# Kernel optimization log

Measured on AMD Instinct MI355X. Metric: run time of the kernel, lower is better.

## Reference

```python
import math
import jax, jax.numpy as jnp
import numpy as np

B, H, S, D = 8, 16, 1024, 64
NEG = -1000000000.0


def setup_inputs() -> dict:
    key = jax.random.key(0)
    kq, kk, kv, km = jax.random.split(key, 4)
    return {
        "query": jax.random.normal(kq, (B, H, S, D), dtype=jnp.float32),
        "key": jax.random.normal(kk, (B, H, S, D), dtype=jnp.float32),
        "value": jax.random.normal(kv, (B, H, S, D), dtype=jnp.float32),
        "mask": jax.random.randint(km, (B, 1, S, S), 0, 2, dtype=jnp.int32),
    }


def reference(query, key, value, mask):
    dk = query.shape[-1]
    # [B,H,S,S] scores
    scores = jnp.einsum("bhqd,bhkd->bhqk", query, key) / math.sqrt(dk)
    valid = mask != 0  # broadcast [B,1,S,S]
    scores = jnp.where(valid, scores, NEG)
    attention = jax.nn.softmax(scores, axis=-1)
    # second masking pass: zero out masked attention weights
    attention = jnp.where(valid, attention, 0.0)
    out = jnp.einsum("bhqk,bhkd->bhqd", attention, value)
    return (out, attention)
```

## Files before the change

kernel.cpp:

```cpp
#include <hip/hip_runtime.h>
#include <stdint.h>


typedef _Float16 half8 __attribute__((ext_vector_type(8)));
typedef _Float16 half4v __attribute__((ext_vector_type(4)));
typedef float floatx4 __attribute__((ext_vector_type(4)));
typedef unsigned short u16;

constexpr int Bc = 8, Hc = 16, Sc = 1024, Dc = 64;
constexpr float NEGV = -1000000000.0f;
constexpr float SCALE = 0.125f;

__device__ inline half8 cvt8(float4 a, float4 b) {
    half8 h;
    h[0] = (_Float16)a.x; h[1] = (_Float16)a.y; h[2] = (_Float16)a.z; h[3] = (_Float16)a.w;
    h[4] = (_Float16)b.x; h[5] = (_Float16)b.y; h[6] = (_Float16)b.z; h[7] = (_Float16)b.w;
    return h;
}

__device__ inline void gll16(const void* g, void* l) {
    __builtin_amdgcn_global_load_lds(
        (const __attribute__((address_space(1))) unsigned int*)g,
        (__attribute__((address_space(3))) unsigned int*)l, 16, 0, 0);
}

__global__ __launch_bounds__(256) void prep_all(
    const float* __restrict__ K, const float* __restrict__ V,
    const int* __restrict__ M,
    _Float16* __restrict__ Kh, _Float16* __restrict__ Vh, u16* __restrict__ MB)
{
    const int bid = blockIdx.x;
    const int t = threadIdx.x;
    if (bid < 2048) {
        const size_t nv = (size_t)Bc * Hc * Sc * Dc / 4;
        for (size_t i = (size_t)bid * 256 + t; i < 2 * nv; i += (size_t)2048 * 256) {
            const bool isK = i < nv;
            const size_t j = isK ? i : i - nv;
            const float4 f = ((const float4*)(isK ? K : V))[j];
            half4v h;
            h[0] = (_Float16)f.x; h[1] = (_Float16)f.y;
            h[2] = (_Float16)f.z; h[3] = (_Float16)f.w;
            *(half4v*)((isK ? Kh : Vh) + j * 4) = h;
        }
    } else {
        const int id = bid - 2048;
        const int qt = id & 63, b = id >> 6;
        const int idx2 = t & 63;
        const int w2 = idx2 >> 4, cc = idx2 & 15;
        const int kbase = cc * 64 + w2 * 16;
#pragma unroll
        for (int it = 0; it < 4; ++it) {
            const int row = it * 4 + (t >> 6);
            const int* mp = M + ((size_t)b * Sc + qt * 16 + row) * Sc + kbase;
            unsigned m = 0;
#pragma unroll
            for (int j4 = 0; j4 < 4; ++j4) {
                const int4 mi = *(const int4*)(mp + j4 * 4);
                m |= (mi.x != 0 ? 1u : 0u) << (j4 * 4 + 0);
                m |= (mi.y != 0 ? 1u : 0u) << (j4 * 4 + 1);
                m |= (mi.z != 0 ? 1u : 0u) << (j4 * 4 + 2);
                m |= (mi.w != 0 ? 1u : 0u) << (j4 * 4 + 3);
            }
            MB[(size_t)(b * 64 + qt) * 1024 + row * 64 + idx2] = (u16)m;
        }
    }
}

__global__ __launch_bounds__(256, 3) void attn15(
    const float* __restrict__ Q,
    const _Float16* __restrict__ Kh, const _Float16* __restrict__ Vh,
    const u16* __restrict__ MB,
    float* __restrict__ Out, float* __restrict__ Attn)
{
    __shared__ __align__(16) unsigned char sh[49664];
    _Float16* p_lds      = (_Float16*)sh;
    unsigned char* stg   = sh + 32768;
    float* redM          = (float*)(sh + 49152);
    float* redS          = (float*)(sh + 49408);

    const int t = threadIdx.x, lane = t & 63, w = t >> 6;
    const int g = lane >> 4, n = lane & 15;
    const int bh = blockIdx.y, b = bh >> 4, qt = blockIdx.x, qtile = qt * 16;

    const unsigned char* KhB = (const unsigned char*)(Kh + (size_t)bh * Sc * Dc);
    const unsigned char* VhB = (const unsigned char*)(Vh + (size_t)bh * Sc * Dc);

    union { uint4 v[2]; u16 h[16]; } mu;
    {
        const u16* mrow = MB + (size_t)(b * 64 + qt) * 1024 + n * 64 + w * 16;
        mu.v[0] = *(const uint4*)&mrow[0];
        mu.v[1] = *(const uint4*)&mrow[8];
    }

    half8 qf0, qf1;
    {
        const float* qr = Q + ((size_t)bh * Sc + qtile + n) * Dc;
        float4 a0 = *(const float4*)&qr[g * 8];
        float4 a1 = *(const float4*)&qr[g * 8 + 4];
        float4 a2 = *(const float4*)&qr[32 + g * 8];
        float4 a3 = *(const float4*)&qr[32 + g * 8 + 4];
        a0.x *= SCALE; a0.y *= SCALE; a0.z *= SCALE; a0.w *= SCALE;
        a1.x *= SCALE; a1.y *= SCALE; a1.z *= SCALE; a1.w *= SCALE;
        a2.x *= SCALE; a2.y *= SCALE; a2.z *= SCALE; a2.w *= SCALE;
        a3.x *= SCALE; a3.y *= SCALE; a3.z *= SCALE; a3.w *= SCALE;
        qf0 = cvt8(a0, a1);
        qf1 = cvt8(a2, a3);
    }

    int koff[2], voff[2];
#pragma unroll
    for (int i = 0; i < 2; ++i) {
        const int G = w * 128 + i * 64 + lane;
        const int row = G >> 3, cb = (G & 7) * 16;
        koff[i] = row * 128 + (cb ^ ((row & 7) << 4));
        const int Gv = (i * 4 + w) * 64 + lane;
        const int st = Gv >> 3, jj = Gv & 7;
        const int jk = jj >> 1, dd8 = jj & 1;
        const int kb = st >> 5, d0 = (st >> 3) & 3, sub = (st >> 2) & 1, gg = st & 3;
        const int kk = kb * 32 + gg * 8 + sub * 4 + jk;
        voff[i] = kk * 128 + (d0 * 16 + dd8 * 8) * 2;
    }

    gll16(KhB + koff[0],        stg + w * 2048);
    gll16(KhB + koff[1],        stg + w * 2048 + 1024);
    gll16(KhB + 8192 + koff[0], stg + 8192 + w * 2048);
    gll16(KhB + 8192 + koff[1], stg + 8192 + w * 2048 + 1024);

    const int rowk = w * 16 + n;
    const int swk = (rowk & 7) << 4;
    float s[64];

#pragma unroll
    for (int c = 0; c < 16; ++c) {
        if (c == 15) { asm volatile("s_waitcnt vmcnt(0)" ::: "memory"); }
        else         { asm volatile("s_waitcnt vmcnt(2)" ::: "memory"); }
        __builtin_amdgcn_sched_barrier(0);
        const unsigned char* buf = stg + (c & 1) * 8192;
        const half8 kf0 = *(const half8*)(buf + rowk * 128 + ((g * 16) ^ swk));
        const half8 kf1 = *(const half8*)(buf + rowk * 128 + ((64 + g * 16) ^ swk));
        floatx4 acc = {0.f, 0.f, 0.f, 0.f};
        acc = __builtin_amdgcn_mfma_f32_16x16x32_f16(kf0, qf0, acc, 0, 0, 0);
        acc = __builtin_amdgcn_mfma_f32_16x16x32_f16(kf1, qf1, acc, 0, 0, 0);
        const unsigned mb = mu.h[c];
#pragma unroll
        for (int r = 0; r < 4; ++r)
            s[c * 4 + r] = ((mb >> (g * 4 + r)) & 1) ? acc[r] : NEGV;
        if (c + 2 < 16) {
            asm volatile("s_waitcnt lgkmcnt(0)" ::: "memory");
            __builtin_amdgcn_sched_barrier(0);
            unsigned char* dst = stg + (c & 1) * 8192 + w * 2048;
            gll16(KhB + (size_t)(c + 2) * 8192 + koff[0], dst);
            gll16(KhB + (size_t)(c + 2) * 8192 + koff[1], dst + 1024);
        }
    }

    float mloc = -3.4e38f;
#pragma unroll
    for (int c = 0; c < 16; ++c) {
        mloc = fmaxf(mloc, fmaxf(fmaxf(s[c * 4], s[c * 4 + 1]),
                                 fmaxf(s[c * 4 + 2], s[c * 4 + 3])));
    }
    mloc = fmaxf(mloc, __shfl_xor(mloc, 16, 64));
    mloc = fmaxf(mloc, __shfl_xor(mloc, 32, 64));
    if (lane < 16) redM[w * 16 + n] = mloc;
    __syncthreads();
    const float mx = fmaxf(fmaxf(redM[n], redM[16 + n]),
                           fmaxf(redM[32 + n], redM[48 + n]));

    gll16(VhB + voff[0],        stg + w * 1024);
    gll16(VhB + voff[1],        stg + (4 + w) * 1024);
    gll16(VhB + 8192 + voff[0], stg + 8192 + w * 1024);
    gll16(VhB + 8192 + voff[1], stg + 8192 + (4 + w) * 1024);

    float s0 = 0.f, s1 = 0.f, s2 = 0.f, s3 = 0.f;
#pragma unroll
    for (int c = 0; c < 16; ++c) {
        const float p0 = __expf(s[c * 4 + 0] - mx);
        const float p1 = __expf(s[c * 4 + 1] - mx);
        const float p2 = __expf(s[c * 4 + 2] - mx);
        const float p3 = __expf(s[c * 4 + 3] - mx);
        s[c * 4 + 0] = p0; s[c * 4 + 1] = p1;
        s[c * 4 + 2] = p2; s[c * 4 + 3] = p3;
        s0 += p0; s1 += p1; s2 += p2; s3 += p3;
    }
    float sloc = (s0 + s1) + (s2 + s3);
    sloc += __shfl_xor(sloc, 16, 64);
    sloc += __shfl_xor(sloc, 32, 64);
    if (lane < 16) redS[w * 16 + n] = sloc;
    __syncthreads();
    const float inv = __builtin_amdgcn_rcpf(redS[n] + redS[16 + n] +
                                            redS[32 + n] + redS[48 + n]);

    const unsigned swzn = (unsigned)((n & 7) << 3);
#pragma unroll
    for (int c = 0; c < 16; ++c) {
        const int col = c * 64 + w * 16 + g * 4;
        half4v hp;
        hp[0] = (_Float16)(s[c * 4 + 0] * inv);
        hp[1] = (_Float16)(s[c * 4 + 1] * inv);
        hp[2] = (_Float16)(s[c * 4 + 2] * inv);
        hp[3] = (_Float16)(s[c * 4 + 3] * inv);
        *(half4v*)&p_lds[n * 1024 + (col ^ swzn)] = hp;
    }
    __syncthreads();

    floatx4 oacc = {0.f, 0.f, 0.f, 0.f};

#pragma unroll
    for (int c = 0; c < 16; ++c) {
        if (c == 15) { asm volatile("s_waitcnt vmcnt(0)" ::: "memory"); }
        else         { asm volatile("s_waitcnt vmcnt(2)" ::: "memory"); }
        __builtin_amdgcn_sched_barrier(0);
        const unsigned vt_base = (unsigned)(uintptr_t)(stg + (c & 1) * 8192);
        __builtin_amdgcn_s_setprio(1);
        const int pc0 = c * 64 + g * 8;
        const half8 pa0 = *(const half8*)&p_lds[n * 1024 + (pc0 ^ swzn)];
        const half8 pa1 = *(const half8*)&p_lds[n * 1024 + ((pc0 + 32) ^ swzn)];
        const unsigned va0 = vt_base + (((unsigned)w * 8 + (unsigned)g) * 64 + (unsigned)n * 4) * 2;
        const unsigned va1 = va0 + 4096;
        half4v r0, r1, r2, r3;
        asm volatile("ds_read_b64_tr_b16 %0, %4\n\t"
                     "ds_read_b64_tr_b16 %1, %4 offset:512\n\t"
                     "ds_read_b64_tr_b16 %2, %5\n\t"
                     "ds_read_b64_tr_b16 %3, %5 offset:512"
                     : "=&v"(r0), "=&v"(r1), "=&v"(r2), "=&v"(r3)
                     : "v"(va0), "v"(va1));
        asm volatile("s_waitcnt lgkmcnt(0)" ::: "memory");
        __builtin_amdgcn_sched_barrier(0);
        if (c + 2 < 16) {
            unsigned char* dst = stg + (c & 1) * 8192;
            gll16(VhB + (size_t)(c + 2) * 8192 + voff[0], dst + w * 1024);
            gll16(VhB + (size_t)(c + 2) * 8192 + voff[1], dst + (4 + w) * 1024);
        }
        half8 vf0, vf1;
        vf0[0] = r0[0]; vf0[1] = r0[1]; vf0[2] = r0[2]; vf0[3] = r0[3];
        vf0[4] = r1[0]; vf0[5] = r1[1]; vf0[6] = r1[2]; vf0[7] = r1[3];
        vf1[0] = r2[0]; vf1[1] = r2[1]; vf1[2] = r2[2]; vf1[3] = r2[3];
        vf1[4] = r3[0]; vf1[5] = r3[1]; vf1[6] = r3[2]; vf1[7] = r3[3];
        oacc = __builtin_amdgcn_mfma_f32_16x16x32_f16(pa0, vf0, oacc, 0, 0, 0);
        oacc = __builtin_amdgcn_mfma_f32_16x16x32_f16(pa1, vf1, oacc, 0, 0, 0);
        __builtin_amdgcn_s_setprio(0);
    }

    const int dcol = w * 16 + n;
    const int qrow = qtile + g * 4;
    float* Ob = Out + (size_t)bh * Sc * Dc;
#pragma unroll
    for (int r = 0; r < 4; ++r) {
        __builtin_nontemporal_store(oacc[r], &Ob[(size_t)(qrow + r) * Dc + dcol]);
    }

    const int row_a = t >> 4, ca = (t & 15) * 4;
    const unsigned swza = (unsigned)((row_a & 7) << 3);
    float* arow = Attn + (size_t)bh * Sc * Sc + (size_t)(qtile + row_a) * Sc;
#pragma unroll
    for (int c = 0; c < 16; ++c) {
        const int col = c * 64 + ca;
        const half4v h = *(const half4v*)&p_lds[row_a * 1024 + (col ^ swza)];
        floatx4 f;
        f[0] = (float)h[0]; f[1] = (float)h[1]; f[2] = (float)h[2]; f[3] = (float)h[3];
        __builtin_nontemporal_store(f, (floatx4*)&arow[col]);
    }
}

__global__ __launch_bounds__(256, 4) void attn_fb(
    const float* __restrict__ Q, const float* __restrict__ K,
    const float* __restrict__ V, const int* __restrict__ M,
    float* __restrict__ Out, float* __restrict__ Attn)
{
    __shared__ __align__(16) unsigned char sh[33280];
    _Float16* p_lds = (_Float16*)sh;
    float*    redM  = (float*)(sh + 32768);
    float*    redS  = (float*)(sh + 33024);

    const int t = threadIdx.x, lane = t & 63, w = t >> 6;
    const int g = lane >> 4, n = lane & 15;
    const int bh = blockIdx.y, b = bh >> 4, qt = blockIdx.x, qtile = qt * 16;
    const int kbase = w * 256;

    half8 qf0, qf1;
    {
        const float* qr = Q + ((size_t)bh * Sc + qtile + n) * Dc;
        float4 a0 = *(const float4*)&qr[g * 8];
        float4 a1 = *(const float4*)&qr[g * 8 + 4];
        float4 a2 = *(const float4*)&qr[32 + g * 8];
        float4 a3 = *(const float4*)&qr[32 + g * 8 + 4];
        a0.x *= SCALE; a0.y *= SCALE; a0.z *= SCALE; a0.w *= SCALE;
        a1.x *= SCALE; a1.y *= SCALE; a1.z *= SCALE; a1.w *= SCALE;
        a2.x *= SCALE; a2.y *= SCALE; a2.z *= SCALE; a2.w *= SCALE;
        a3.x *= SCALE; a3.y *= SCALE; a3.z *= SCALE; a3.w *= SCALE;
        qf0 = cvt8(a0, a1);
        qf1 = cvt8(a2, a3);
    }

    float s[64];
#pragma unroll
    for (int kt = 0; kt < 16; ++kt) {
        const int key = kbase + kt * 16 + n;
        const float* kr = K + ((size_t)bh * Sc + key) * Dc;
        const half8 kf0 = cvt8(*(const float4*)&kr[g * 8], *(const float4*)&kr[g * 8 + 4]);
        const half8 kf1 = cvt8(*(const float4*)&kr[32 + g * 8], *(const float4*)&kr[32 + g * 8 + 4]);
        floatx4 acc = {0.f, 0.f, 0.f, 0.f};
        acc = __builtin_amdgcn_mfma_f32_16x16x32_f16(kf0, qf0, acc, 0, 0, 0);
        acc = __builtin_amdgcn_mfma_f32_16x16x32_f16(kf1, qf1, acc, 0, 0, 0);
        const int4 mi = *(const int4*)(M + ((size_t)b * Sc + qtile + n) * Sc +
                                       kbase + kt * 16 + g * 4);
        s[kt * 4 + 0] = mi.x ? acc[0] : NEGV;
        s[kt * 4 + 1] = mi.y ? acc[1] : NEGV;
        s[kt * 4 + 2] = mi.z ? acc[2] : NEGV;
        s[kt * 4 + 3] = mi.w ? acc[3] : NEGV;
    }

    float mloc = -3.4e38f;
#pragma unroll
    for (int kt = 0; kt < 16; ++kt)
        mloc = fmaxf(mloc, fmaxf(fmaxf(s[kt * 4], s[kt * 4 + 1]),
                                 fmaxf(s[kt * 4 + 2], s[kt * 4 + 3])));
    mloc = fmaxf(mloc, __shfl_xor(mloc, 16, 64));
    mloc = fmaxf(mloc, __shfl_xor(mloc, 32, 64));
    if (lane < 16) redM[w * 16 + n] = mloc;
    __syncthreads();
    const float mx = fmaxf(fmaxf(redM[n], redM[16 + n]),
                           fmaxf(redM[32 + n], redM[48 + n]));
    float sloc = 0.f;
#pragma unroll
    for (int kt = 0; kt < 16; ++kt) {
#pragma unroll
        for (int r = 0; r < 4; ++r) {
            const float p = __expf(s[kt * 4 + r] - mx);
            s[kt * 4 + r] = p;
            sloc += p;
        }
    }
    sloc += __shfl_xor(sloc, 16, 64);
    sloc += __shfl_xor(sloc, 32, 64);
    if (lane < 16) redS[w * 16 + n] = sloc;
    __syncthreads();
    const float inv = __builtin_amdgcn_rcpf(redS[n] + redS[16 + n] +
                                            redS[32 + n] + redS[48 + n]);

    const unsigned swzn = (unsigned)((n & 7) << 3);
#pragma unroll
    for (int kt = 0; kt < 16; ++kt) {
        const int col = kbase + kt * 16 + g * 4;
        half4v hp;
        hp[0] = (_Float16)(s[kt * 4 + 0] * inv);
        hp[1] = (_Float16)(s[kt * 4 + 1] * inv);
        hp[2] = (_Float16)(s[kt * 4 + 2] * inv);
        hp[3] = (_Float16)(s[kt * 4 + 3] * inv);
        *(half4v*)&p_lds[n * 1024 + (col ^ swzn)] = hp;
    }
    __syncthreads();

    const int dcol_v = w * 16 + n;
    const int row_a = t >> 4, ca = (t & 15) * 4;
    const unsigned swza = (unsigned)((row_a & 7) << 3);
    float* arow = Attn + (size_t)bh * Sc * Sc + (size_t)(qtile + row_a) * Sc;
    floatx4 oacc = {0.f, 0.f, 0.f, 0.f};
#pragma unroll
    for (int i = 0; i < 32; ++i) {
        if ((i & 1) == 0) {
            const int col = (i >> 1) * 64 + ca;
            const half4v h = *(const half4v*)&p_lds[row_a * 1024 + (col ^ swza)];
            float4 f;
            f.x = (float)h[0]; f.y = (float)h[1]; f.z = (float)h[2]; f.w = (float)h[3];
            *(float4*)&arow[col] = f;
        }
        const half8 pa = *(const half8*)&p_lds[n * 1024 + ((i * 32 + g * 8) ^ swzn)];
        half8 vf;
#pragma unroll
        for (int j = 0; j < 8; ++j)
            vf[j] = (_Float16)V[((size_t)bh * Sc + i * 32 + g * 8 + j) * Dc + dcol_v];
        oacc = __builtin_amdgcn_mfma_f32_16x16x32_f16(pa, vf, oacc, 0, 0, 0);
    }
    const int qrow = qtile + g * 4;
    float* Ob = Out + (size_t)bh * Sc * Dc;
#pragma unroll
    for (int r = 0; r < 4; ++r)
        Ob[(size_t)(qrow + r) * Dc + dcol_v] = oacc[r];
}

extern "C" void kernel_launch(void* const* d_in, const int* in_sizes, int n_in,
                              void* d_out, int out_size, void* d_ws, size_t ws_size,
                              hipStream_t stream) {
    const float* Q = (const float*)d_in[0];
    const float* K = (const float*)d_in[1];
    const float* V = (const float*)d_in[2];
    const int*   M = (const int*)d_in[3];

    float* Out  = (float*)d_out;
    float* Attn = (float*)d_out + (size_t)Bc * Hc * Sc * Dc;

    const size_t nEl = (size_t)Bc * Hc * Sc * Dc;
    const size_t needed = nEl * 2 * 2 + (size_t)Bc * 64 * 1024 * 2;

    dim3 grid(Sc / 16, Bc * Hc);
    dim3 block(256);

    if (ws_size >= needed) {
        _Float16* Kh = (_Float16*)d_ws;
        _Float16* Vh = Kh + nEl;
        u16*      MB = (u16*)(Vh + nEl);
        prep_all<<<2560, 256, 0, stream>>>(K, V, M, Kh, Vh, MB);
        attn15<<<grid, block, 0, stream>>>(Q, Kh, Vh, MB, Out, Attn);
    } else {
        attn_fb<<<grid, block, 0, stream>>>(Q, K, V, M, Out, Attn);
    }
}
```

Baseline: 204.3 us.

## Halve P buffer in LDS to raise occupancy from 3 to 4 blocks

The normalized probability tile is now staged in LDS in two 512-column halves instead of the full 1024 columns. This cuts shared memory from about 49.6KB to 33KB so launch bounds can request 4 blocks per CU. The first half of the attention output is cached in registers before the second half overwrites the buffer. __syncthreads is also replaced with a lighter lgkmcnt-wait plus barrier. The cost is an extra barrier round, more register pressure from the cached half, and less overlap between the attention writes and the PV loop.

```diff
diff --git a/kernel.cpp b/kernel.cpp
--- a/kernel.cpp
+++ b/kernel.cpp
@@ -22,6 +22,12 @@
     __builtin_amdgcn_global_load_lds(
         (const __attribute__((address_space(1))) unsigned int*)g,
         (__attribute__((address_space(3))) unsigned int*)l, 16, 0, 0);
+}
+
+__device__ inline void bar_lgkm() {
+    asm volatile("s_waitcnt lgkmcnt(0)" ::: "memory");
+    __builtin_amdgcn_s_barrier();
+    __builtin_amdgcn_sched_barrier(0);
 }
 
 __global__ __launch_bounds__(256) void prep_all(
@@ -66,17 +72,17 @@
     }
 }
 
-__global__ __launch_bounds__(256, 3) void attn15(
+__global__ __launch_bounds__(256, 4) void attn16(
     const float* __restrict__ Q,
     const _Float16* __restrict__ Kh, const _Float16* __restrict__ Vh,
     const u16* __restrict__ MB,
     float* __restrict__ Out, float* __restrict__ Attn)
 {
-    __shared__ __align__(16) unsigned char sh[49664];
+    __shared__ __align__(16) unsigned char sh[33280];
     _Float16* p_lds      = (_Float16*)sh;
-    unsigned char* stg   = sh + 32768;
-    float* redM          = (float*)(sh + 49152);
-    float* redS          = (float*)(sh + 49408);
+    unsigned char* stg   = sh + 16384;
+    float* redM          = (float*)(sh + 32768);
+    float* redS          = (float*)(sh + 33024);
 
     const int t = threadIdx.x, lane = t & 63, w = t >> 6;
     const int g = lane >> 4, n = lane & 15;
@@ -163,7 +169,7 @@
     mloc = fmaxf(mloc, __shfl_xor(mloc, 16, 64));
     mloc = fmaxf(mloc, __shfl_xor(mloc, 32, 64));
     if (lane < 16) redM[w * 16 + n] = mloc;
-    __syncthreads();
+    bar_lgkm();
     const float mx = fmaxf(fmaxf(redM[n], redM[16 + n]),
                            fmaxf(redM[32 + n], redM[48 + n]));
 
@@ -187,59 +193,75 @@
     sloc += __shfl_xor(sloc, 16, 64);
     sloc += __shfl_xor(sloc, 32, 64);
     if (lane < 16) redS[w * 16 + n] = sloc;
-    __syncthreads();
+    bar_lgkm();
     const float inv = __builtin_amdgcn_rcpf(redS[n] + redS[16 + n] +
                                             redS[32 + n] + redS[48 + n]);
 
     const unsigned swzn = (unsigned)((n & 7) << 3);
-#pragma unroll
-    for (int c = 0; c < 16; ++c) {
-        const int col = c * 64 + w * 16 + g * 4;
-        half4v hp;
-        hp[0] = (_Float16)(s[c * 4 + 0] * inv);
-        hp[1] = (_Float16)(s[c * 4 + 1] * inv);
-        hp[2] = (_Float16)(s[c * 4 + 2] * inv);
-        hp[3] = (_Float16)(s[c * 4 + 3] * inv);
-        *(half4v*)&p_lds[n * 1024 + (col ^ swzn)] = hp;
-    }
-    __syncthreads();
-
+    const int row_a = t >> 4, ca = (t & 15) * 4;
+    const unsigned swza = (unsigned)((row_a & 7) << 3);
     floatx4 oacc = {0.f, 0.f, 0.f, 0.f};
-
-#pragma unroll
-    for (int c = 0; c < 16; ++c) {
-        if (c == 15) { asm volatile("s_waitcnt vmcnt(0)" ::: "memory"); }
-        else         { asm volatile("s_waitcnt vmcnt(2)" ::: "memory"); }
-        __builtin_amdgcn_sched_barrier(0);
-        const unsigned vt_base = (unsigned)(uintptr_t)(stg + (c & 1) * 8192);
-        __builtin_amdgcn_s_setprio(1);
-        const int pc0 = c * 64 + g * 8;
-        const half8 pa0 = *(const half8*)&p_lds[n * 1024 + (pc0 ^ swzn)];
-        const half8 pa1 = *(const half8*)&p_lds[n * 1024 + ((pc0 + 32) ^ swzn)];
-        const unsigned va0 = vt_base + (((unsigned)w * 8 + (unsigned)g) * 64 + (unsigned)n * 4) * 2;
-        const unsigned va1 = va0 + 4096;
-        half4v r0, r1, r2, r3;
-        asm volatile("ds_read_b64_tr_b16 %0, %4\n\t"
-                     "ds_read_b64_tr_b16 %1, %4 offset:512\n\t"
-                     "ds_read_b64_tr_b16 %2, %5\n\t"
-                     "ds_read_b64_tr_b16 %3, %5 offset:512"
-                     : "=&v"(r0), "=&v"(r1), "=&v"(r2), "=&v"(r3)
-                     : "v"(va0), "v"(va1));
-        asm volatile("s_waitcnt lgkmcnt(0)" ::: "memory");
-        __builtin_amdgcn_sched_barrier(0);
-        if (c + 2 < 16) {
-            unsigned char* dst = stg + (c & 1) * 8192;
-            gll16(VhB + (size_t)(c + 2) * 8192 + voff[0], dst + w * 1024);
-            gll16(VhB + (size_t)(c + 2) * 8192 + voff[1], dst + (4 + w) * 1024);
-        }
-        half8 vf0, vf1;
-        vf0[0] = r0[0]; vf0[1] = r0[1]; vf0[2] = r0[2]; vf0[3] = r0[3];
-        vf0[4] = r1[0]; vf0[5] = r1[1]; vf0[6] = r1[2]; vf0[7] = r1[3];
-        vf1[0] = r2[0]; vf1[1] = r2[1]; vf1[2] = r2[2]; vf1[3] = r2[3];
-        vf1[4] = r3[0]; vf1[5] = r3[1]; vf1[6] = r3[2]; vf1[7] = r3[3];
-        oacc = __builtin_amdgcn_mfma_f32_16x16x32_f16(pa0, vf0, oacc, 0, 0, 0);
-        oacc = __builtin_amdgcn_mfma_f32_16x16x32_f16(pa1, vf1, oacc, 0, 0, 0);
-        __builtin_amdgcn_s_setprio(0);
+    half4v acache[8];
+
+#pragma unroll
+    for (int h = 0; h < 2; ++h) {
+        if (h == 1) bar_lgkm();
+#pragma unroll
+        for (int c8 = 0; c8 < 8; ++c8) {
+            const int c = h * 8 + c8;
+            const int col_h = c8 * 64 + w * 16 + g * 4;
+            half4v hp;
+            hp[0] = (_Float16)(s[c * 4 + 0] * inv);
+            hp[1] = (_Float16)(s[c * 4 + 1] * inv);
+            hp[2] = (_Float16)(s[c * 4 + 2] * inv);
+            hp[3] = (_Float16)(s[c * 4 + 3] * inv);
+            *(half4v*)&p_lds[n * 512 + (col_h ^ swzn)] = hp;
+        }
+        bar_lgkm();
+
+#pragma unroll
+        for (int c8 = 0; c8 < 8; ++c8) {
+            const int c = h * 8 + c8;
+            if (c == 15) { asm volatile("s_waitcnt vmcnt(0)" ::: "memory"); }
+            else         { asm volatile("s_waitcnt vmcnt(2)" ::: "memory"); }
+            __builtin_amdgcn_sched_barrier(0);
+            const unsigned vt_base = (unsigned)(uintptr_t)(stg + (c & 1) * 8192);
+            __builtin_amdgcn_s_setprio(1);
+            const int pc0 = c8 * 64 + g * 8;
+            const half8 pa0 = *(const half8*)&p_lds[n * 512 + (pc0 ^ swzn)];
+            const half8 pa1 = *(const half8*)&p_lds[n * 512 + ((pc0 + 32) ^ swzn)];
+            const unsigned va0 = vt_base +
+                (((unsigned)w * 8 + (unsigned)g) * 64 + (unsigned)n * 4) * 2;
+            const unsigned va1 = va0 + 4096;
+            half4v r0, r1, r2, r3;
+            asm volatile("ds_read_b64_tr_b16 %0, %4\n\t"
+                         "ds_read_b64_tr_b16 %1, %4 offset:512\n\t"
+                         "ds_read_b64_tr_b16 %2, %5\n\t"
+                         "ds_read_b64_tr_b16 %3, %5 offset:512"
+                         : "=&v"(r0), "=&v"(r1), "=&v"(r2), "=&v"(r3)
+                         : "v"(va0), "v"(va1));
+            asm volatile("s_waitcnt lgkmcnt(0)" ::: "memory");
+            __builtin_amdgcn_sched_barrier(0);
+            if (c + 2 < 16) {
+                unsigned char* dst = stg + (c & 1) * 8192;
+                gll16(VhB + (size_t)(c + 2) * 8192 + voff[0], dst + w * 1024);
+                gll16(VhB + (size_t)(c + 2) * 8192 + voff[1], dst + (4 + w) * 1024);
+            }
+            half8 vf0, vf1;
+            vf0[0] = r0[0]; vf0[1] = r0[1]; vf0[2] = r0[2]; vf0[3] = r0[3];
+            vf0[4] = r1[0]; vf0[5] = r1[1]; vf0[6] = r1[2]; vf0[7] = r1[3];
+            vf1[0] = r2[0]; vf1[1] = r2[1]; vf1[2] = r2[2]; vf1[3] = r2[3];
+            vf1[4] = r3[0]; vf1[5] = r3[1]; vf1[6] = r3[2]; vf1[7] = r3[3];
+            oacc = __builtin_amdgcn_mfma_f32_16x16x32_f16(pa0, vf0, oacc, 0, 0, 0);
+            oacc = __builtin_amdgcn_mfma_f32_16x16x32_f16(pa1, vf1, oacc, 0, 0, 0);
+            __builtin_amdgcn_s_setprio(0);
+        }
+        if (h == 0) {
+#pragma unroll
+            for (int c8 = 0; c8 < 8; ++c8) {
+                acache[c8] = *(const half4v*)&p_lds[row_a * 512 + ((c8 * 64 + ca) ^ swza)];
+            }
+        }
     }
 
     const int dcol = w * 16 + n;
@@ -249,17 +271,20 @@
     for (int r = 0; r < 4; ++r) {
         __builtin_nontemporal_store(oacc[r], &Ob[(size_t)(qrow + r) * Dc + dcol]);
     }
-
-    const int row_a = t >> 4, ca = (t & 15) * 4;
-    const unsigned swza = (unsigned)((row_a & 7) << 3);
     float* arow = Attn + (size_t)bh * Sc * Sc + (size_t)(qtile + row_a) * Sc;
 #pragma unroll
-    for (int c = 0; c < 16; ++c) {
-        const int col = c * 64 + ca;
-        const half4v h = *(const half4v*)&p_lds[row_a * 1024 + (col ^ swza)];
+    for (int c8 = 0; c8 < 8; ++c8) {
+        const half4v hh = acache[c8];
         floatx4 f;
-        f[0] = (float)h[0]; f[1] = (float)h[1]; f[2] = (float)h[2]; f[3] = (float)h[3];
-        __builtin_nontemporal_store(f, (floatx4*)&arow[col]);
+        f[0] = (float)hh[0]; f[1] = (float)hh[1]; f[2] = (float)hh[2]; f[3] = (float)hh[3];
+        __builtin_nontemporal_store(f, (floatx4*)&arow[c8 * 64 + ca]);
+    }
+#pragma unroll
+    for (int c8 = 0; c8 < 8; ++c8) {
+        const half4v hh = *(const half4v*)&p_lds[row_a * 512 + ((c8 * 64 + ca) ^ swza)];
+        floatx4 f;
+        f[0] = (float)hh[0]; f[1] = (float)hh[1]; f[2] = (float)hh[2]; f[3] = (float)hh[3];
+        __builtin_nontemporal_store(f, (floatx4*)&arow[512 + c8 * 64 + ca]);
     }
 }
 
@@ -402,7 +427,7 @@
         _Float16* Vh = Kh + nEl;
         u16*      MB = (u16*)(Vh + nEl);
         prep_all<<<2560, 256, 0, stream>>>(K, V, M, Kh, Vh, MB);
-        attn15<<<grid, block, 0, stream>>>(Q, Kh, Vh, MB, Out, Attn);
+        attn16<<<grid, block, 0, stream>>>(Q, Kh, Vh, MB, Out, Attn);
     } else {
         attn_fb<<<grid, block, 0, stream>>>(Q, K, V, M, Out, Attn);
     }
```

Result: faster. 194.5 us (-4.8%).
